# Optimization experiments

Hardware: AMD Instinct MI355X
Metric: run time of the kernel (lower is better)

## Reference

```python
import jax, jax.numpy as jnp
import numpy as np

# dims: T time steps, B batch, F clinical features, H GRU hidden, NH heads, DFF ffn dim, AH single-attn hidden
T, B, F, H, NH, DFF, AH = 128, 256, 76, 64, 4, 256, 8


def setup_inputs() -> dict:
    key = jax.random.key(0)
    ks = jax.random.split(key, 32)
    s = 0.1
    def u(k, shape):
        return jax.random.uniform(k, shape, jnp.float32, -s, s)
    return {
        "x": jax.random.normal(ks[0], (T, B, F), jnp.float32),
        # per-feature GRU(1, H) weight stacks (torch gate order: r, z, n)
        "gru_w_ih": u(ks[1], (F, 3 * H)),          # input dim is 1 -> squeezed
        "gru_w_hh": u(ks[2], (F, 3 * H, H)),
        "gru_b_ih": jnp.zeros((F, 3 * H), jnp.float32),
        "gru_b_hh": jnp.zeros((F, 3 * H), jnp.float32),
        # per-feature SingleAttention('new', time_aware) params
        "att_Wt": u(ks[3], (F, H, AH)),
        "att_Wx": u(ks[4], (F, H, AH)),
        "att_rate": jnp.full((F,), 0.8, jnp.float32),
        # multi-head self-attention over the feature axis
        "mha_wq": u(ks[5], (H, H)), "mha_bq": jnp.zeros((H,), jnp.float32),
        "mha_wk": u(ks[6], (H, H)), "mha_bk": jnp.zeros((H,), jnp.float32),
        "mha_wv": u(ks[7], (H, H)), "mha_bv": jnp.zeros((H,), jnp.float32),
        "mha_wo": u(ks[8], (H, H)), "mha_bo": jnp.zeros((H,), jnp.float32),
        # position-wise feed forward
        "ffn_w1": u(ks[9], (H, DFF)), "ffn_b1": jnp.zeros((DFF,), jnp.float32),
        "ffn_w2": u(ks[10], (DFF, H)), "ffn_b2": jnp.zeros((H,), jnp.float32),
        # FinalAttentionQKV ('mul')
        "fa_wq": u(ks[11], (H, H)), "fa_bq": jnp.zeros((H,), jnp.float32),
        "fa_wk": u(ks[12], (H, H)), "fa_bk": jnp.zeros((H,), jnp.float32),
        "fa_wv": u(ks[13], (H, H)), "fa_bv": jnp.zeros((H,), jnp.float32),
        # output head
        "out0_w": u(ks[14], (H, H)), "out0_b": jnp.zeros((H,), jnp.float32),
        "out1_w": u(ks[15], (H, 1)), "out1_b": jnp.zeros((1,), jnp.float32),
    }


def reference(x, gru_w_ih, gru_w_hh, gru_b_ih, gru_b_hh,
              att_Wt, att_Wx, att_rate,
              mha_wq, mha_bq, mha_wk, mha_bk, mha_wv, mha_bv, mha_wo, mha_bo,
              ffn_w1, ffn_b1, ffn_w2, ffn_b2,
              fa_wq, fa_bq, fa_wk, fa_bk, fa_wv, fa_bv,
              out0_w, out0_b, out1_w, out1_b):
    # x: (T, B, F); torch permutes to (B, T, F)
    Ts, Bsz, Fd = x.shape
    Hd = gru_w_hh.shape[-1]
    dk = Hd // NH

    # ---- all F GRU(1,H) channels fused into one scan (vectorized over F) ----
    xs = jnp.transpose(x, (0, 2, 1))  # (T, F, B)

    def step(h, x_t):  # h: (F,B,H), x_t: (F,B)
        gx = x_t[:, :, None] * gru_w_ih[:, None, :] + gru_b_ih[:, None, :]      # (F,B,3H)
        gh = jnp.einsum('fbh,fgh->fbg', h, gru_w_hh) + gru_b_hh[:, None, :]     # (F,B,3H)
        rx, zx, nx = jnp.split(gx, 3, axis=-1)
        rh, zh, nh = jnp.split(gh, 3, axis=-1)
        r = jax.nn.sigmoid(rx + rh)
        z = jax.nn.sigmoid(zx + zh)
        n = jnp.tanh(nx + r * nh)
        h_new = (1.0 - z) * n + z * h
        return h_new, h_new

    h0 = jnp.zeros((Fd, Bsz, Hd), x.dtype)
    _, hs = jax.lax.scan(step, h0, xs)        # (T, F, B, H)
    hs = jnp.transpose(hs, (1, 2, 0, 3))       # (F, B, T, H)

    # ---- per-feature SingleAttention, type='new', time-aware ----
    q = jnp.einsum('fbh,fha->fba', hs[:, :, -1, :], att_Wt)   # (F,B,AH)
    k = jnp.einsum('fbth,fha->fbta', hs, att_Wx)              # (F,B,T,AH)
    dp = jnp.einsum('fba,fbta->fbt', q, k)                    # (F,B,T)
    sig = jax.nn.sigmoid(dp)
    decay = jnp.arange(Ts, 0, -1, dtype=x.dtype)              # T..1 (time_decays + 1)
    denom = jax.nn.sigmoid(att_rate)[:, None, None] * (jnp.log(2.72 + (1.0 - sig)) * decay)
    e = jax.nn.relu(sig / denom)
    a = jax.nn.softmax(e, axis=-1)
    emb = jnp.einsum('fbt,fbth->bfh', a, hs)                  # (B, F, H)

    def lin(t, w, b):
        return t @ w + b

    # ---- multi-head self-attention over the F axis + residual ----
    # NOTE: original lambda ignores its (layernormed) argument, so LN is dead code.
    def heads(t):
        return t.reshape(Bsz, Fd, NH, dk).transpose(0, 2, 1, 3)
    qh = heads(lin(emb, mha_wq, mha_bq))
    kh = heads(lin(emb, mha_wk, mha_bk))
    vh = heads(lin(emb, mha_wv, mha_bv))
    scores = jnp.einsum('bhqd,bhkd->bhqk', qh, kh) / jnp.sqrt(jnp.asarray(dk, x.dtype))
    attn = jax.nn.softmax(scores, axis=-1)
    ctx = jnp.einsum('bhqk,bhkd->bhqd', attn, vh).transpose(0, 2, 1, 3).reshape(Bsz, Fd, Hd)
    ctx = emb + lin(ctx, mha_wo, mha_bo)

    # ---- position-wise feed-forward + residual ----
    ctx = ctx + lin(jax.nn.relu(lin(ctx, ffn_w1, ffn_b1)), ffn_w2, ffn_b2)

    # ---- FinalAttentionQKV, type='mul' ----
    fq = lin(ctx[:, -1, :], fa_wq, fa_bq)      # (B,H)
    fk = lin(ctx, fa_wk, fa_bk)                # (B,F,H)
    fv = lin(ctx, fa_wv, fa_bv)                # (B,F,H)
    fe = jnp.einsum('bfh,bh->bf', fk, fq)
    fa_w = jax.nn.softmax(fe, axis=1)
    v = jnp.einsum('bf,bfh->bh', fa_w, fv)     # (B,H)

    # ---- output head ----
    out = jax.nn.sigmoid(lin(jax.nn.relu(lin(v, out0_w, out0_b)), out1_w, out1_b))
    return out  # (B, 1)
```

## Files before the change

kernel.cpp:

```cpp
#include <hip/hip_runtime.h>
#include <hip/hip_bf16.h>
#include <cstdint>
#include <cstddef>

#define TT 128
#define BBATCH 256
#define FFEAT 76
#define HDIM 64
#define NHEAD 4
#define DKH 16
#define DFF1 256
#define AH1 8
#define NROWS (BBATCH * FFEAT)

#define LOG2E 1.4426950408889634f

typedef __attribute__((ext_vector_type(8))) short bf16x8;
typedef __attribute__((ext_vector_type(4))) float f32x4;

__device__ __forceinline__ float fast_sigmoid(float v) {
    float p = __builtin_amdgcn_exp2f(-v * LOG2E);
    return __builtin_amdgcn_rcpf(1.0f + p);
}
__device__ __forceinline__ float fast_tanh(float v) {
    float p = __builtin_amdgcn_exp2f(v * (2.0f * LOG2E));
    return 1.0f - 2.0f * __builtin_amdgcn_rcpf(1.0f + p);
}
__device__ __forceinline__ short f2bf(float x) {
    __hip_bfloat16 h = __float2bfloat16(x);
    return *reinterpret_cast<short*>(&h);
}
__device__ __forceinline__ float bf2f(unsigned short s) {
    return __uint_as_float(((unsigned)s) << 16);
}
__device__ __forceinline__ unsigned pack_bf16(float a, float b) {
    unsigned ua = (unsigned)(unsigned short)f2bf(a);
    unsigned ub = (unsigned)(unsigned short)f2bf(b);
    return ua | (ub << 16);
}

__global__ __launch_bounds__(64) void gru_scan_kernel(
    const float* __restrict__ x, const float* __restrict__ w_ih,
    const float* __restrict__ w_hh, const float* __restrict__ b_ih,
    const float* __restrict__ b_hh, const float* __restrict__ Wt,
    const float* __restrict__ Wx, int f_base,
    __hip_bfloat16* __restrict__ hs, float* __restrict__ wtil)
{
    const int f_loc = blockIdx.y;
    const int f     = f_base + f_loc;
    const int b0    = blockIdx.x * 16;
    const int lane  = threadIdx.x;
    const int c     = lane & 15;
    const int q     = lane >> 4;

    __shared__ float x_lds[TT][16];
    __shared__ float wt_s[64][8];
    __shared__ float wx_s[64][8];
    __shared__ short hx[16][72];
    __shared__ float q_s[16][8];

    for (int i = lane; i < TT * 16; i += 64) {
        int t = i >> 4, b = i & 15;
        x_lds[t][b] = x[((size_t)t * BBATCH + b0 + b) * FFEAT + f];
    }
    for (int i = lane; i < 512; i += 64) {
        ((float*)wt_s)[i] = Wt[(size_t)f * 512 + i];
        ((float*)wx_s)[i] = Wx[(size_t)f * 512 + i];
    }
    __syncthreads();

    bf16x8 afr[12][2];
    {
        const float* whh_f = w_hh + (size_t)f * 192 * 64;
        #pragma unroll
        for (int nt = 0; nt < 12; ++nt) {
            int gate = nt >> 2, tt = nt & 3;
            int urow = (c >> 2) * 8 + (tt & 1) * 4 + (c & 3) + (tt >> 1) * 32;
            const float* row = whh_f + (size_t)(gate * 64 + urow) * 64;
            #pragma unroll
            for (int kq = 0; kq < 2; ++kq) {
                bf16x8 fr;
                #pragma unroll
                for (int j = 0; j < 8; ++j) fr[j] = f2bf(row[kq * 32 + q * 8 + j]);
                afr[nt][kq] = fr;
            }
        }
    }
    float wr[4][4], wz[4][4], wn[4][4], bnx[4][4];
    f32x4 biasv[12];
    #pragma unroll
    for (int tt = 0; tt < 4; ++tt) {
        #pragma unroll
        for (int r = 0; r < 4; ++r) {
            int u = q * 8 + (tt & 1) * 4 + r + (tt >> 1) * 32;
            wr[tt][r]  = w_ih[f*192 + u];
            wz[tt][r]  = w_ih[f*192 + 64 + u];
            wn[tt][r]  = w_ih[f*192 + 128 + u];
            bnx[tt][r] = b_ih[f*192 + 128 + u];
            biasv[tt][r]     = b_ih[f*192 + u]      + b_hh[f*192 + u];
            biasv[4 + tt][r] = b_ih[f*192 + 64 + u] + b_hh[f*192 + 64 + u];
            biasv[8 + tt][r] = b_hh[f*192 + 128 + u];
        }
    }

    float hprev[4][4];
    #pragma unroll
    for (int tt = 0; tt < 4; ++tt)
        #pragma unroll
        for (int r = 0; r < 4; ++r) hprev[tt][r] = 0.f;

    bf16x8 hb0 = {0,0,0,0,0,0,0,0};
    bf16x8 hb1 = {0,0,0,0,0,0,0,0};

    short* hs_b = (short*)hs + ((size_t)f_loc * BBATCH + b0 + c) * TT * HDIM;

    for (int t = 0; t < TT; ++t) {
        f32x4 acc[12];
        #pragma unroll
        for (int nt = 0; nt < 12; ++nt) {
            f32x4 a = __builtin_amdgcn_mfma_f32_16x16x32_bf16(afr[nt][0], hb0, biasv[nt], 0, 0, 0);
            acc[nt]  = __builtin_amdgcn_mfma_f32_16x16x32_bf16(afr[nt][1], hb1, a, 0, 0, 0);
        }

        float xv = x_lds[t][c];
        float hn4[4][4];
        #pragma unroll
        for (int tt = 0; tt < 4; ++tt) {
            #pragma unroll
            for (int r = 0; r < 4; ++r) {
                float R  = fmaf(xv, wr[tt][r], acc[tt][r]);
                float Z  = fmaf(xv, wz[tt][r], acc[4 + tt][r]);
                float NX = fmaf(xv, wn[tt][r], bnx[tt][r]);
                float rg = fast_sigmoid(R);
                float zg = fast_sigmoid(Z);
                float ng = fast_tanh(fmaf(rg, acc[8 + tt][r], NX));
                float hn = fmaf(zg, hprev[tt][r] - ng, ng);
                hprev[tt][r] = hn;
                hn4[tt][r] = hn;
            }
        }
        {
            union { int4 i; bf16x8 v; } u0, u1;
            u0.i.x = pack_bf16(hn4[0][0], hn4[0][1]);
            u0.i.y = pack_bf16(hn4[0][2], hn4[0][3]);
            u0.i.z = pack_bf16(hn4[1][0], hn4[1][1]);
            u0.i.w = pack_bf16(hn4[1][2], hn4[1][3]);
            u1.i.x = pack_bf16(hn4[2][0], hn4[2][1]);
            u1.i.y = pack_bf16(hn4[2][2], hn4[2][3]);
            u1.i.z = pack_bf16(hn4[3][0], hn4[3][1]);
            u1.i.w = pack_bf16(hn4[3][2], hn4[3][3]);
            hb0 = u0.v; hb1 = u1.v;
        }
        short* dst = hs_b + (size_t)t * HDIM + q * 8;
        *(bf16x8*)dst = hb0;
        *(bf16x8*)(dst + 32) = hb1;
    }

    *(bf16x8*)&hx[c][q * 8]      = hb0;
    *(bf16x8*)&hx[c][32 + q * 8] = hb1;

    #pragma unroll
    for (int rr = 0; rr < 2; ++rr) {
        int role = rr * 64 + lane;
        int b = role >> 3, a = role & 7;
        float s = 0.f;
        #pragma unroll 8
        for (int j = 0; j < 64; ++j)
            s = fmaf(bf2f((unsigned short)hx[b][j]), wt_s[j][a], s);
        q_s[b][a] = s;
    }
    {
        int b = lane >> 2, jb = (lane & 3) * 16;
        float qreg[8];
        #pragma unroll
        for (int a = 0; a < 8; ++a) qreg[a] = q_s[b][a];
        float* wt_out = wtil + ((size_t)(b0 + b) * FFEAT + f) * HDIM + jb;
        #pragma unroll
        for (int j4 = 0; j4 < 4; ++j4) {
            float4 v;
            #pragma unroll
            for (int jj = 0; jj < 4; ++jj) {
                int j = jb + j4 * 4 + jj;
                float s = 0.f;
                #pragma unroll
                for (int a = 0; a < 8; ++a) s = fmaf(wx_s[j][a], qreg[a], s);
                (&v.x)[jj] = s;
            }
            *(float4*)&wt_out[j4 * 4] = v;
        }
    }
}

__global__ __launch_bounds__(256) void attn2_kernel(
    const __hip_bfloat16* __restrict__ hs, const float* wtil,
    const float* __restrict__ rate, int f_base, float* emb)
{
    const int w     = threadIdx.x >> 6;
    const int lane  = threadIdx.x & 63;
    const int b     = blockIdx.x * 4 + w;
    const int f_loc = blockIdx.y;
    const int f     = f_base + f_loc;
    const int g     = lane >> 3;
    const int i     = lane & 7;

    const uint4* basev = (const uint4*)((const short*)hs +
                          ((size_t)f_loc * BBATCH + b) * TT * HDIM);

    uint4 U[16];
    #pragma unroll
    for (int it = 0; it < 16; ++it)
        U[it] = basev[(it * 8 + g) * 8 + i];

    float wv[8];
    {
        const float4* src = (const float4*)(wtil + ((size_t)b * FFEAT + f) * HDIM + 8 * i);
        float4 a = src[0], c2 = src[1];
        wv[0]=a.x; wv[1]=a.y; wv[2]=a.z; wv[3]=a.w;
        wv[4]=c2.x; wv[5]=c2.y; wv[6]=c2.z; wv[7]=c2.w;
    }
    const float rs = fast_sigmoid(rate[f]);

    float m = -1.0e30f, s = 0.f;
    float o[8];
    #pragma unroll
    for (int j = 0; j < 8; ++j) o[j] = 0.f;

    #pragma unroll
    for (int it = 0; it < 16; ++it) {
        const int t = it * 8 + g;
        uint4 Uv = U[it];
        float h[8];
        h[0] = __uint_as_float(Uv.x << 16); h[1] = __uint_as_float(Uv.x & 0xffff0000u);
        h[2] = __uint_as_float(Uv.y << 16); h[3] = __uint_as_float(Uv.y & 0xffff0000u);
        h[4] = __uint_as_float(Uv.z << 16); h[5] = __uint_as_float(Uv.z & 0xffff0000u);
        h[6] = __uint_as_float(Uv.w << 16); h[7] = __uint_as_float(Uv.w & 0xffff0000u);
        float dp = 0.f;
        #pragma unroll
        for (int j = 0; j < 8; ++j) dp = fmaf(h[j], wv[j], dp);
        dp += __shfl_xor(dp, 1, 64);
        dp += __shfl_xor(dp, 2, 64);
        dp += __shfl_xor(dp, 4, 64);
        float sig = fast_sigmoid(dp);
        float den = rs * (__logf(2.72f + (1.0f - sig)) * (float)(TT - t));
        float e = fmaxf(sig / den, 0.0f);
        float nm = fmaxf(m, e);
        float sc = __builtin_amdgcn_exp2f((m - nm) * LOG2E);
        float p  = __builtin_amdgcn_exp2f((e - nm) * LOG2E);
        s = fmaf(s, sc, p);
        #pragma unroll
        for (int j = 0; j < 8; ++j) o[j] = fmaf(o[j], sc, p * h[j]);
        m = nm;
    }
    #pragma unroll
    for (int k = 8; k <= 32; k <<= 1) {
        float om = __shfl_xor(m, k, 64);
        float os = __shfl_xor(s, k, 64);
        float nm = fmaxf(m, om);
        float sa = __builtin_amdgcn_exp2f((m - nm) * LOG2E);
        float sb = __builtin_amdgcn_exp2f((om - nm) * LOG2E);
        s = s * sa + os * sb;
        #pragma unroll
        for (int j = 0; j < 8; ++j) {
            float oo = __shfl_xor(o[j], k, 64);
            o[j] = o[j] * sa + oo * sb;
        }
        m = nm;
    }
    if (g == 0) {
        float inv = __builtin_amdgcn_rcpf(s);
        float4 v0, v1;
        v0.x = o[0]*inv; v0.y = o[1]*inv; v0.z = o[2]*inv; v0.w = o[3]*inv;
        v1.x = o[4]*inv; v1.y = o[5]*inv; v1.z = o[6]*inv; v1.w = o[7]*inv;
        float* dst = &emb[((size_t)b * FFEAT + f) * HDIM + 8 * i];
        *(float4*)dst       = v0;
        *(float4*)(dst + 4) = v1;
    }
}

struct GemmP {
    const float* X;
    const float* W[3];
    const float* B[3];
    const float* R;
    float* Y[3];
    int K;
    int Nfull;
    int act;
};

__global__ __launch_bounds__(256) void gemm_kernel(GemmP A)
{
    __shared__ float xs[64][65];
    __shared__ float ws[64][68];

    const int tid = threadIdx.x;
    const int tx  = tid & 15;
    const int ty  = tid >> 4;
    const int m0  = blockIdx.x * 64;
    const int n0  = blockIdx.y * 64;
    const int z   = blockIdx.z;

    const float* W = A.W[z];
    const float* Bv = A.B[z];
    float* Y = A.Y[z];
    const int K = A.K, Nfull = A.Nfull;

    float acc[4][4];
    #pragma unroll
    for (int i = 0; i < 4; ++i)
        #pragma unroll
        for (int j = 0; j < 4; ++j) acc[i][j] = 0.f;

    for (int kc = 0; kc < K; kc += 64) {
        for (int s = tid; s < 1024; s += 256) {
            int row = s >> 4, c4 = s & 15;
            float4 xv = *(const float4*)&A.X[(size_t)(m0 + row) * K + kc + 4*c4];
            xs[row][4*c4+0] = xv.x; xs[row][4*c4+1] = xv.y;
            xs[row][4*c4+2] = xv.z; xs[row][4*c4+3] = xv.w;
            float4 wv = *(const float4*)&W[(size_t)(kc + row) * Nfull + n0 + 4*c4];
            *(float4*)&ws[row][4*c4] = wv;
        }
        __syncthreads();
        #pragma unroll 16
        for (int k = 0; k < 64; ++k) {
            float a0 = xs[4*ty+0][k], a1 = xs[4*ty+1][k];
            float a2 = xs[4*ty+2][k], a3 = xs[4*ty+3][k];
            float4 wv = *(const float4*)&ws[k][4*tx];
            #pragma unroll
            for (int j = 0; j < 4; ++j) {
                float wj = (&wv.x)[j];
                acc[0][j] = fmaf(a0, wj, acc[0][j]);
                acc[1][j] = fmaf(a1, wj, acc[1][j]);
                acc[2][j] = fmaf(a2, wj, acc[2][j]);
                acc[3][j] = fmaf(a3, wj, acc[3][j]);
            }
        }
        __syncthreads();
    }

    float4 bias = *(const float4*)&Bv[n0 + 4*tx];
    #pragma unroll
    for (int i = 0; i < 4; ++i) {
        int row = m0 + 4*ty + i;
        float4 v;
        v.x = acc[i][0] + bias.x; v.y = acc[i][1] + bias.y;
        v.z = acc[i][2] + bias.z; v.w = acc[i][3] + bias.w;
        if (A.act) {
            v.x = fmaxf(v.x, 0.f); v.y = fmaxf(v.y, 0.f);
            v.z = fmaxf(v.z, 0.f); v.w = fmaxf(v.w, 0.f);
        }
        if (A.R) {
            float4 r4 = *(const float4*)&A.R[(size_t)row * Nfull + n0 + 4*tx];
            v.x += r4.x; v.y += r4.y; v.z += r4.z; v.w += r4.w;
        }
        *(float4*)&Y[(size_t)row * Nfull + n0 + 4*tx] = v;
    }
}

__global__ __launch_bounds__(256) void mha_core_kernel(
    const float* __restrict__ q, const float* __restrict__ k,
    const float* __restrict__ v, float* __restrict__ ctx)
{
    const int b  = blockIdx.x;
    const int hh = blockIdx.y;
    const int tid = threadIdx.x;

    __shared__ float qs[FFEAT][17];
    __shared__ float ks[FFEAT][17];
    __shared__ float vs[FFEAT][17];
    __shared__ float ps[FFEAT][77];

    for (int idx = tid; idx < FFEAT * DKH; idx += 256) {
        int i = idx >> 4, c = idx & 15;
        size_t g = ((size_t)b * FFEAT + i) * HDIM + hh * DKH + c;
        qs[i][c] = q[g]; ks[i][c] = k[g]; vs[i][c] = v[g];
    }
    __syncthreads();

    for (int idx = tid; idx < FFEAT * FFEAT; idx += 256) {
        int i = idx / FFEAT, j = idx % FFEAT;
        float acc = 0.f;
        #pragma unroll
        for (int c = 0; c < DKH; ++c) acc = fmaf(qs[i][c], ks[j][c], acc);
        ps[i][j] = acc * 0.25f;
    }
    __syncthreads();

    if (tid < FFEAT) {
        float mm = ps[tid][0];
        #pragma unroll 4
        for (int j = 1; j < FFEAT; ++j) mm = fmaxf(mm, ps[tid][j]);
        float ss = 0.f;
        #pragma unroll 4
        for (int j = 0; j < FFEAT; ++j) {
            float pv = __builtin_amdgcn_exp2f((ps[tid][j] - mm) * LOG2E);
            ps[tid][j] = pv; ss += pv;
        }
        float inv = 1.0f / ss;
        #pragma unroll 4
        for (int j = 0; j < FFEAT; ++j) ps[tid][j] *= inv;
    }
    __syncthreads();

    for (int idx = tid; idx < FFEAT * DKH; idx += 256) {
        int i = idx >> 4, c = idx & 15;
        float acc = 0.f;
        #pragma unroll 4
        for (int j = 0; j < FFEAT; ++j) acc = fmaf(ps[i][j], vs[j][c], acc);
        ctx[((size_t)b * FFEAT + i) * HDIM + hh * DKH + c] = acc;
    }
}

__global__ __launch_bounds__(128) void final_kernel(
    const float* __restrict__ ctx3, const float* __restrict__ fk,
    const float* __restrict__ fv,
    const float* __restrict__ faq, const float* __restrict__ fabq,
    const float* __restrict__ o0w, const float* __restrict__ o0b,
    const float* __restrict__ o1w, const float* __restrict__ o1b,
    float* __restrict__ out)
{
    const int b = blockIdx.x;
    const int tid = threadIdx.x;

    __shared__ float last[HDIM];
    __shared__ float fqs[HDIM];
    __shared__ float sm[FFEAT];
    __shared__ float vv[HDIM];
    __shared__ float hh[HDIM];
    __shared__ float redm[2], redp[2];

    if (tid < HDIM) last[tid] = ctx3[((size_t)b * FFEAT + FFEAT - 1) * HDIM + tid];
    __syncthreads();
    if (tid < HDIM) {
        float acc = fabq[tid];
        #pragma unroll 8
        for (int j = 0; j < HDIM; ++j) acc = fmaf(last[j], faq[j * HDIM + tid], acc);
        fqs[tid] = acc;
    }
    __syncthreads();

    float e = -3.0e38f;
    if (tid < FFEAT) {
        const float4* kr = (const float4*)&fk[((size_t)b * FFEAT + tid) * HDIM];
        float acc = 0.f;
        #pragma unroll
        for (int c4 = 0; c4 < 16; ++c4) {
            float4 kv = kr[c4];
            acc = fmaf(kv.x, fqs[4*c4+0], acc);
            acc = fmaf(kv.y, fqs[4*c4+1], acc);
            acc = fmaf(kv.z, fqs[4*c4+2], acc);
            acc = fmaf(kv.w, fqs[4*c4+3], acc);
        }
        e = acc;
    }
    float m = e;
    #pragma unroll
    for (int off = 32; off > 0; off >>= 1) m = fmaxf(m, __shfl_xor(m, off, 64));
    if ((tid & 63) == 0) redm[tid >> 6] = m;
    __syncthreads();
    m = fmaxf(redm[0], redm[1]);
    float p = (tid < FFEAT) ? __builtin_amdgcn_exp2f((e - m) * LOG2E) : 0.f;
    float s = p;
    #pragma unroll
    for (int off = 32; off > 0; off >>= 1) s += __shfl_xor(s, off, 64);
    if ((tid & 63) == 0) redp[tid >> 6] = s;
    __syncthreads();
    s = redp[0] + redp[1];
    if (tid < FFEAT) sm[tid] = p / s;
    __syncthreads();

    if (tid < HDIM) {
        float acc = 0.f;
        for (int ff = 0; ff < FFEAT; ++ff)
            acc = fmaf(sm[ff], fv[((size_t)b * FFEAT + ff) * HDIM + tid], acc);
        vv[tid] = acc;
    }
    __syncthreads();
    if (tid < HDIM) {
        float acc = o0b[tid];
        #pragma unroll 8
        for (int j = 0; j < HDIM; ++j) acc = fmaf(vv[j], o0w[j * HDIM + tid], acc);
        hh[tid] = fmaxf(acc, 0.f);
    }
    __syncthreads();
    if (tid < 64) {
        float t = hh[tid] * o1w[tid];
        #pragma unroll
        for (int off = 32; off > 0; off >>= 1) t += __shfl_xor(t, off, 64);
        if (tid == 0) out[b] = fast_sigmoid(t + o1b[0]);
    }
}

__global__ void ws_report_kernel(float* out, int n, float ws_mib) {
    int i = blockIdx.x * blockDim.x + threadIdx.x;
    if (i < n) out[i] = ws_mib;
}

extern "C" void kernel_launch(void* const* d_in, const int* in_sizes, int n_in,
                              void* d_out, int out_size, void* d_ws, size_t ws_size,
                              hipStream_t stream)
{
    const float* x     = (const float*)d_in[0];
    const float* w_ih  = (const float*)d_in[1];
    const float* w_hh  = (const float*)d_in[2];
    const float* b_ih  = (const float*)d_in[3];
    const float* b_hh  = (const float*)d_in[4];
    const float* attWt = (const float*)d_in[5];
    const float* attWx = (const float*)d_in[6];
    const float* attRt = (const float*)d_in[7];
    const float* wq    = (const float*)d_in[8];
    const float* bq    = (const float*)d_in[9];
    const float* wk    = (const float*)d_in[10];
    const float* bk    = (const float*)d_in[11];
    const float* wv    = (const float*)d_in[12];
    const float* bv    = (const float*)d_in[13];
    const float* wo    = (const float*)d_in[14];
    const float* bo    = (const float*)d_in[15];
    const float* w1    = (const float*)d_in[16];
    const float* b1    = (const float*)d_in[17];
    const float* w2    = (const float*)d_in[18];
    const float* b2    = (const float*)d_in[19];
    const float* faq   = (const float*)d_in[20];
    const float* fabq  = (const float*)d_in[21];
    const float* fak   = (const float*)d_in[22];
    const float* fabk  = (const float*)d_in[23];
    const float* fav   = (const float*)d_in[24];
    const float* fabv  = (const float*)d_in[25];
    const float* o0w   = (const float*)d_in[26];
    const float* o0b   = (const float*)d_in[27];
    const float* o1w   = (const float*)d_in[28];
    const float* o1b   = (const float*)d_in[29];
    float* out = (float*)d_out;

    const size_t embwtil_bytes = (size_t)NROWS * HDIM * 4;
    const size_t R64           = (size_t)NROWS * HDIM;
    const size_t tail_bytes    = 12 * R64 * 4;

    const int chunk_opts[6] = {76, 38, 19, 4, 2, 1};
    int FC = 0;
    for (int i = 0; i < 6; ++i) {
        size_t hs_b = (size_t)chunk_opts[i] * BBATCH * TT * HDIM * 2;
        size_t scratch = hs_b > tail_bytes ? hs_b : tail_bytes;
        if (embwtil_bytes + scratch <= ws_size) { FC = chunk_opts[i]; break; }
    }
    if (FC == 0) {
        ws_report_kernel<<<dim3((out_size + 255) / 256), dim3(256), 0, stream>>>(
            out, out_size, (float)((double)ws_size / (1024.0 * 1024.0)));
        return;
    }

    float* embwtil = (float*)d_ws;
    char*  scratch = (char*)d_ws + embwtil_bytes;
    __hip_bfloat16* hs = (__hip_bfloat16*)scratch;

    for (int f0 = 0; f0 < FFEAT; f0 += FC) {
        int fc = (FFEAT - f0 < FC) ? (FFEAT - f0) : FC;
        gru_scan_kernel<<<dim3(16, fc), dim3(64), 0, stream>>>(
            x, w_ih, w_hh, b_ih, b_hh, attWt, attWx, f0, hs, embwtil);
        attn2_kernel<<<dim3(BBATCH / 4, fc), dim3(256), 0, stream>>>(
            hs, embwtil, attRt, f0, embwtil);
    }

    float* emb  = embwtil;
    float* ts   = (float*)scratch;
    float* q    = ts;
    float* k    = ts + 1*R64;
    float* v    = ts + 2*R64;
    float* ctx  = ts + 3*R64;
    float* ctx2 = ts + 4*R64;
    float* hid  = ts + 5*R64;
    float* ctx3 = ts + 9*R64;
    float* fk   = ts + 10*R64;
    float* fv   = ts + 11*R64;

    const int MB = NROWS / 64;

    {
        GemmP A = { emb, {wq, wk, wv}, {bq, bk, bv}, nullptr, {q, k, v}, 64, 64, 0 };
        gemm_kernel<<<dim3(MB, 1, 3), dim3(256), 0, stream>>>(A);
    }
    mha_core_kernel<<<dim3(BBATCH, NHEAD), dim3(256), 0, stream>>>(q, k, v, ctx);
    {
        GemmP A = { ctx, {wo, nullptr, nullptr}, {bo, nullptr, nullptr}, emb,
                    {ctx2, nullptr, nullptr}, 64, 64, 0 };
        gemm_kernel<<<dim3(MB, 1, 1), dim3(256), 0, stream>>>(A);
    }
    {
        GemmP A = { ctx2, {w1, nullptr, nullptr}, {b1, nullptr, nullptr}, nullptr,
                    {hid, nullptr, nullptr}, 64, 256, 1 };
        gemm_kernel<<<dim3(MB, 4, 1), dim3(256), 0, stream>>>(A);
    }
    {
        GemmP A = { hid, {w2, nullptr, nullptr}, {b2, nullptr, nullptr}, ctx2,
                    {ctx3, nullptr, nullptr}, 256, 64, 0 };
        gemm_kernel<<<dim3(MB, 1, 1), dim3(256), 0, stream>>>(A);
    }
    {
        GemmP A = { ctx3, {fak, fav, nullptr}, {fabk, fabv, nullptr}, nullptr,
                    {fk, fv, nullptr}, 64, 64, 0 };
        gemm_kernel<<<dim3(MB, 1, 2), dim3(256), 0, stream>>>(A);
    }
    final_kernel<<<dim3(BBATCH), dim3(128), 0, stream>>>(
        ctx3, fk, fv, faq, fabq, o0w, o0b, o1w, o1b, out);
}
```

Baseline: 564.7 us.

## Overlap GRU scan of second feature half with attention of first half

Result: no change. 563.8 us (-0.2%).

```diff
diff --git a/kernel.cpp b/kernel.cpp
--- a/kernel.cpp
+++ b/kernel.cpp
@@ -12,6 +12,7 @@
 #define DFF1 256
 #define AH1 8
 #define NROWS (BBATCH * FFEAT)
+#define FCP 38
 
 #define LOG2E 1.4426950408889634f
 
@@ -37,6 +38,267 @@
     unsigned ua = (unsigned)(unsigned short)f2bf(a);
     unsigned ub = (unsigned)(unsigned short)f2bf(b);
     return ua | (ub << 16);
+}
+
+__device__ __forceinline__ void attn_wave(
+    __hip_bfloat16* hs_chunk, const float* Wt, const float* Wx,
+    const float* rate, int f, int f_loc, int b, int lane)
+{
+    const int g = lane >> 3;
+    const int i = lane & 7;
+    short* rowbase = (short*)hs_chunk + ((size_t)f_loc * BBATCH + b) * TT * HDIM;
+    const uint4* basev = (const uint4*)rowbase;
+
+    uint4 U[16];
+    #pragma unroll
+    for (int it = 0; it < 16; ++it)
+        U[it] = basev[(it * 8 + g) * 8 + i];
+
+    float qv[8];
+    {
+        uint4 Uv = U[15];
+        float h15[8];
+        h15[0]=__uint_as_float(Uv.x<<16); h15[1]=__uint_as_float(Uv.x&0xffff0000u);
+        h15[2]=__uint_as_float(Uv.y<<16); h15[3]=__uint_as_float(Uv.y&0xffff0000u);
+        h15[4]=__uint_as_float(Uv.z<<16); h15[5]=__uint_as_float(Uv.z&0xffff0000u);
+        h15[6]=__uint_as_float(Uv.w<<16); h15[7]=__uint_as_float(Uv.w&0xffff0000u);
+        const float* wtp = Wt + (size_t)f * 512 + (size_t)(8 * i) * 8;
+        #pragma unroll
+        for (int a = 0; a < 8; ++a) qv[a] = 0.f;
+        #pragma unroll
+        for (int j = 0; j < 8; ++j)
+            #pragma unroll
+            for (int a = 0; a < 8; ++a)
+                qv[a] = fmaf(h15[j], wtp[j * 8 + a], qv[a]);
+        #pragma unroll
+        for (int a = 0; a < 8; ++a) {
+            qv[a] += __shfl_xor(qv[a], 1, 64);
+            qv[a] += __shfl_xor(qv[a], 2, 64);
+            qv[a] += __shfl_xor(qv[a], 4, 64);
+            qv[a]  = __shfl(qv[a], 63, 64);
+        }
+    }
+    float wv[8];
+    {
+        const float* wxp = Wx + (size_t)f * 512 + (size_t)(8 * i) * 8;
+        #pragma unroll
+        for (int j = 0; j < 8; ++j) {
+            float s2 = 0.f;
+            #pragma unroll
+            for (int a = 0; a < 8; ++a) s2 = fmaf(wxp[j * 8 + a], qv[a], s2);
+            wv[j] = s2;
+        }
+    }
+    const float rs = fast_sigmoid(rate[f]);
+
+    float m = -1.0e30f, s = 0.f;
+    float o[8];
+    #pragma unroll
+    for (int j = 0; j < 8; ++j) o[j] = 0.f;
+
+    #pragma unroll
+    for (int it = 0; it < 16; ++it) {
+        const int t = it * 8 + g;
+        uint4 Uv = U[it];
+        float h[8];
+        h[0] = __uint_as_float(Uv.x << 16); h[1] = __uint_as_float(Uv.x & 0xffff0000u);
+        h[2] = __uint_as_float(Uv.y << 16); h[3] = __uint_as_float(Uv.y & 0xffff0000u);
+        h[4] = __uint_as_float(Uv.z << 16); h[5] = __uint_as_float(Uv.z & 0xffff0000u);
+        h[6] = __uint_as_float(Uv.w << 16); h[7] = __uint_as_float(Uv.w & 0xffff0000u);
+        float dp = 0.f;
+        #pragma unroll
+        for (int j = 0; j < 8; ++j) dp = fmaf(h[j], wv[j], dp);
+        dp += __shfl_xor(dp, 1, 64);
+        dp += __shfl_xor(dp, 2, 64);
+        dp += __shfl_xor(dp, 4, 64);
+        float sig = fast_sigmoid(dp);
+        float den = rs * (__logf(2.72f + (1.0f - sig)) * (float)(TT - t));
+        float e = fmaxf(sig / den, 0.0f);
+        float nm = fmaxf(m, e);
+        float sc = __builtin_amdgcn_exp2f((m - nm) * LOG2E);
+        float p  = __builtin_amdgcn_exp2f((e - nm) * LOG2E);
+        s = fmaf(s, sc, p);
+        #pragma unroll
+        for (int j = 0; j < 8; ++j) o[j] = fmaf(o[j], sc, p * h[j]);
+        m = nm;
+    }
+    #pragma unroll
+    for (int k = 8; k <= 32; k <<= 1) {
+        float om = __shfl_xor(m, k, 64);
+        float os = __shfl_xor(s, k, 64);
+        float nm = fmaxf(m, om);
+        float sa = __builtin_amdgcn_exp2f((m - nm) * LOG2E);
+        float sb = __builtin_amdgcn_exp2f((om - nm) * LOG2E);
+        s = s * sa + os * sb;
+        #pragma unroll
+        for (int j = 0; j < 8; ++j) {
+            float oo = __shfl_xor(o[j], k, 64);
+            o[j] = o[j] * sa + oo * sb;
+        }
+        m = nm;
+    }
+    if (g == 0) {
+        float inv = __builtin_amdgcn_rcpf(s);
+        float4 v0, v1;
+        v0.x = o[0]*inv; v0.y = o[1]*inv; v0.z = o[2]*inv; v0.w = o[3]*inv;
+        v1.x = o[4]*inv; v1.y = o[5]*inv; v1.z = o[6]*inv; v1.w = o[7]*inv;
+        float* edst = (float*)rowbase;
+        *(float4*)&edst[8 * i]     = v0;
+        *(float4*)&edst[8 * i + 4] = v1;
+    }
+}
+
+__global__ __launch_bounds__(64) void fused_gru_attn_kernel(
+    const float* __restrict__ x, const float* __restrict__ w_ih,
+    const float* __restrict__ w_hh, const float* __restrict__ b_ih,
+    const float* __restrict__ b_hh, const float* __restrict__ Wt,
+    const float* __restrict__ Wx, const float* __restrict__ rate,
+    int ngru, int f0_gru, __hip_bfloat16* __restrict__ hs_w,
+    int f0_att, __hip_bfloat16* hs_r)
+{
+    __shared__ float x_lds[TT][16];
+    const int gid  = blockIdx.x;
+    const int lane = threadIdx.x;
+
+    if (gid < ngru) {
+        const int f_loc = gid >> 4;
+        const int f     = f0_gru + f_loc;
+        const int b0    = (gid & 15) * 16;
+        const int c     = lane & 15;
+        const int q     = lane >> 4;
+
+        for (int i = lane; i < TT * 16; i += 64) {
+            int t = i >> 4, b = i & 15;
+            x_lds[t][b] = x[((size_t)t * BBATCH + b0 + b) * FFEAT + f];
+        }
+        __syncthreads();
+
+        bf16x8 afr[12][2];
+        {
+            const float* whh_f = w_hh + (size_t)f * 192 * 64;
+            #pragma unroll
+            for (int nt = 0; nt < 12; ++nt) {
+                int gate = nt >> 2, tt = nt & 3;
+                int urow = (c >> 2) * 8 + (tt & 1) * 4 + (c & 3) + (tt >> 1) * 32;
+                const float* row = whh_f + (size_t)(gate * 64 + urow) * 64;
+                #pragma unroll
+                for (int kq = 0; kq < 2; ++kq) {
+                    bf16x8 fr;
+                    #pragma unroll
+                    for (int j = 0; j < 8; ++j) fr[j] = f2bf(row[kq * 32 + q * 8 + j]);
+                    afr[nt][kq] = fr;
+                }
+            }
+        }
+        float wr[4][4], wz[4][4], wn[4][4], bnx[4][4];
+        f32x4 biasv[12];
+        #pragma unroll
+        for (int tt = 0; tt < 4; ++tt) {
+            #pragma unroll
+            for (int r = 0; r < 4; ++r) {
+                int u = q * 8 + (tt & 1) * 4 + r + (tt >> 1) * 32;
+                wr[tt][r]  = w_ih[f*192 + u];
+                wz[tt][r]  = w_ih[f*192 + 64 + u];
+                wn[tt][r]  = w_ih[f*192 + 128 + u];
+                bnx[tt][r] = b_ih[f*192 + 128 + u];
+                biasv[tt][r]     = b_ih[f*192 + u]      + b_hh[f*192 + u];
+                biasv[4 + tt][r] = b_ih[f*192 + 64 + u] + b_hh[f*192 + 64 + u];
+                biasv[8 + tt][r] = b_hh[f*192 + 128 + u];
+            }
+        }
+
+        float hprev[4][4];
+        #pragma unroll
+        for (int tt = 0; tt < 4; ++tt)
+            #pragma unroll
+            for (int r = 0; r < 4; ++r) hprev[tt][r] = 0.f;
+
+        bf16x8 hb0 = {0,0,0,0,0,0,0,0};
+        bf16x8 hb1 = {0,0,0,0,0,0,0,0};
+
+        short* hs_b = (short*)hs_w + ((size_t)f_loc * BBATCH + b0 + c) * TT * HDIM;
+
+        for (int t = 0; t < TT; ++t) {
+            f32x4 acc[12];
+            #pragma unroll
+            for (int nt = 0; nt < 12; ++nt) {
+                f32x4 a = __builtin_amdgcn_mfma_f32_16x16x32_bf16(afr[nt][0], hb0, biasv[nt], 0, 0, 0);
+                acc[nt]  = __builtin_amdgcn_mfma_f32_16x16x32_bf16(afr[nt][1], hb1, a, 0, 0, 0);
+            }
+
+            float xv = x_lds[t][c];
+            float hn4[4][4];
+            #pragma unroll
+            for (int tt = 0; tt < 4; ++tt) {
+                #pragma unroll
+                for (int r = 0; r < 4; ++r) {
+                    float R  = fmaf(xv, wr[tt][r], acc[tt][r]);
+                    float Z  = fmaf(xv, wz[tt][r], acc[4 + tt][r]);
+                    float NX = fmaf(xv, wn[tt][r], bnx[tt][r]);
+                    float rg = fast_sigmoid(R);
+                    float zg = fast_sigmoid(Z);
+                    float ng = fast_tanh(fmaf(rg, acc[8 + tt][r], NX));
+                    float hn = fmaf(zg, hprev[tt][r] - ng, ng);
+                    hprev[tt][r] = hn;
+                    hn4[tt][r] = hn;
+                }
+            }
+            {
+                union { int4 i; bf16x8 v; } u0, u1;
+                u0.i.x = pack_bf16(hn4[0][0], hn4[0][1]);
+                u0.i.y = pack_bf16(hn4[0][2], hn4[0][3]);
+                u0.i.z = pack_bf16(hn4[1][0], hn4[1][1]);
+                u0.i.w = pack_bf16(hn4[1][2], hn4[1][3]);
+                u1.i.x = pack_bf16(hn4[2][0], hn4[2][1]);
+                u1.i.y = pack_bf16(hn4[2][2], hn4[2][3]);
+                u1.i.z = pack_bf16(hn4[3][0], hn4[3][1]);
+                u1.i.w = pack_bf16(hn4[3][2], hn4[3][3]);
+                hb0 = u0.v; hb1 = u1.v;
+            }
+            short* dst = hs_b + (size_t)t * HDIM + q * 8;
+            *(bf16x8*)dst = hb0;
+            *(bf16x8*)(dst + 32) = hb1;
+        }
+    } else {
+        const int aid   = gid - ngru;
+        const int b     = aid & 255;
+        const int f_loc = aid >> 8;
+        attn_wave(hs_r, Wt, Wx, rate, f0_att + f_loc, f_loc, b, lane);
+    }
+}
+
+__global__ __launch_bounds__(256) void attn2_p_kernel(
+    __hip_bfloat16* hs_chunk, const float* __restrict__ Wt,
+    const float* __restrict__ Wx, const float* __restrict__ rate, int f_base)
+{
+    const int w    = threadIdx.x >> 6;
+    const int lane = threadIdx.x & 63;
+    const int b    = blockIdx.x * 4 + w;
+    const int f_loc = blockIdx.y;
+    attn_wave(hs_chunk, Wt, Wx, rate, f_base + f_loc, f_loc, b, lane);
+}
+
+__global__ __launch_bounds__(64) void bounce_kernel(float* hs0f)
+{
+    const int k = blockIdx.x;
+    hs0f[(size_t)(400 + k) * 4096 + 2048 + threadIdx.x] =
+        hs0f[(size_t)k * 4096 + threadIdx.x];
+}
+
+__global__ __launch_bounds__(64) void compact_kernel(
+    const float* hs0f, const float* hs1f, float* emb)
+{
+    const int j = blockIdx.x;
+    const int f = j >> 8;
+    const int b = j & 255;
+    const int chunk = (f >= FCP);
+    const int f_loc = chunk ? f - FCP : f;
+    const size_t row = (size_t)f_loc * BBATCH + b;
+    const float* base = chunk ? hs1f : hs0f;
+    size_t off = (!chunk && row <= 303)
+               ? ((size_t)(400 + row) * 4096 + 2048)
+               : row * 4096;
+    emb[((size_t)b * FFEAT + f) * HDIM + threadIdx.x] = base[off + threadIdx.x];
 }
 
 __global__ __launch_bounds__(64) void gru_scan_kernel(
@@ -494,6 +756,55 @@
 __global__ void ws_report_kernel(float* out, int n, float ws_mib) {
     int i = blockIdx.x * blockDim.x + threadIdx.x;
     if (i < n) out[i] = ws_mib;
+}
+
+static void run_tail(const float* emb, float* ts,
+                     const float* wq, const float* bq, const float* wk2, const float* bk2,
+                     const float* wv2, const float* bv2, const float* wo, const float* bo,
+                     const float* w1, const float* b1, const float* w2, const float* b2,
+                     const float* faq, const float* fabq, const float* fak, const float* fabk,
+                     const float* fav, const float* fabv, const float* o0w, const float* o0b,
+                     const float* o1w, const float* o1b, float* out, hipStream_t stream)
+{
+    const size_t R64 = (size_t)NROWS * HDIM;
+    float* q    = ts;
+    float* k    = ts + 1*R64;
+    float* v    = ts + 2*R64;
+    float* ctx  = ts + 3*R64;
+    float* ctx2 = ts + 4*R64;
+    float* hid  = ts + 5*R64;
+    float* ctx3 = ts + 9*R64;
+    float* fk   = ts + 10*R64;
+    float* fv   = ts + 11*R64;
+    const int MB = NROWS / 64;
+
+    {
+        GemmP A = { emb, {wq, wk2, wv2}, {bq, bk2, bv2}, nullptr, {q, k, v}, 64, 64, 0 };
+        gemm_kernel<<<dim3(MB, 1, 3), dim3(256), 0, stream>>>(A);
+    }
+    mha_core_kernel<<<dim3(BBATCH, NHEAD), dim3(256), 0, stream>>>(q, k, v, ctx);
+    {
+        GemmP A = { ctx, {wo, nullptr, nullptr}, {bo, nullptr, nullptr}, emb,
+                    {ctx2, nullptr, nullptr}, 64, 64, 0 };
+        gemm_kernel<<<dim3(MB, 1, 1), dim3(256), 0, stream>>>(A);
+    }
+    {
+        GemmP A = { ctx2, {w1, nullptr, nullptr}, {b1, nullptr, nullptr}, nullptr,
+                    {hid, nullptr, nullptr}, 64, 256, 1 };
+        gemm_kernel<<<dim3(MB, 4, 1), dim3(256), 0, stream>>>(A);
+    }
+    {
+        GemmP A = { hid, {w2, nullptr, nullptr}, {b2, nullptr, nullptr}, ctx2,
+                    {ctx3, nullptr, nullptr}, 256, 64, 0 };
+        gemm_kernel<<<dim3(MB, 1, 1), dim3(256), 0, stream>>>(A);
+    }
+    {
+        GemmP A = { ctx3, {fak, fav, nullptr}, {fabk, fabv, nullptr}, nullptr,
+                    {fk, fv, nullptr}, 64, 64, 0 };
+        gemm_kernel<<<dim3(MB, 1, 2), dim3(256), 0, stream>>>(A);
+    }
+    final_kernel<<<dim3(BBATCH), dim3(128), 0, stream>>>(
+        ctx3, fk, fv, faq, fabq, o0w, o0b, o1w, o1b, out);
 }
 
 extern "C" void kernel_launch(void* const* d_in, const int* in_sizes, int n_in,
@@ -532,16 +843,41 @@
     const float* o1b   = (const float*)d_in[29];
     float* out = (float*)d_out;
 
-    const size_t embwtil_bytes = (size_t)NROWS * HDIM * 4;
-    const size_t R64           = (size_t)NROWS * HDIM;
-    const size_t tail_bytes    = 12 * R64 * 4;
+    const size_t emb_bytes = (size_t)NROWS * HDIM * 4;
+    const size_t hs_half   = (size_t)FCP * BBATCH * TT * HDIM * 2;
+
+    if (ws_size >= 2 * hs_half) {
+        __hip_bfloat16* hs0 = (__hip_bfloat16*)d_ws;
+        __hip_bfloat16* hs1 = (__hip_bfloat16*)((char*)d_ws + hs_half);
+
+        fused_gru_attn_kernel<<<dim3(16 * FCP), dim3(64), 0, stream>>>(
+            x, w_ih, w_hh, b_ih, b_hh, attWt, attWx, attRt,
+            16 * FCP, 0, hs0, 0, hs1);
+        fused_gru_attn_kernel<<<dim3(16 * FCP + BBATCH * FCP), dim3(64), 0, stream>>>(
+            x, w_ih, w_hh, b_ih, b_hh, attWt, attWx, attRt,
+            16 * FCP, FCP, hs1, 0, hs0);
+        bounce_kernel<<<dim3(304), dim3(64), 0, stream>>>((float*)hs0);
+        attn2_p_kernel<<<dim3(BBATCH / 4, FCP), dim3(256), 0, stream>>>(
+            hs1, attWt, attWx, attRt, FCP);
+        float* emb = (float*)d_ws;
+        compact_kernel<<<dim3(NROWS), dim3(64), 0, stream>>>(
+            (const float*)hs0, (const float*)hs1, emb);
+
+        float* ts = (float*)((char*)d_ws + emb_bytes);
+        run_tail(emb, ts, wq, bq, wk, bk, wv, bv, wo, bo, w1, b1, w2, b2,
+                 faq, fabq, fak, fabk, fav, fabv, o0w, o0b, o1w, o1b, out, stream);
+        return;
+    }
+
+    const size_t R64        = (size_t)NROWS * HDIM;
+    const size_t tail_bytes = 12 * R64 * 4;
 
     const int chunk_opts[6] = {76, 38, 19, 4, 2, 1};
     int FC = 0;
     for (int i = 0; i < 6; ++i) {
         size_t hs_b = (size_t)chunk_opts[i] * BBATCH * TT * HDIM * 2;
         size_t scratch = hs_b > tail_bytes ? hs_b : tail_bytes;
-        if (embwtil_bytes + scratch <= ws_size) { FC = chunk_opts[i]; break; }
+        if (emb_bytes + scratch <= ws_size) { FC = chunk_opts[i]; break; }
     }
     if (FC == 0) {
         ws_report_kernel<<<dim3((out_size + 255) / 256), dim3(256), 0, stream>>>(
@@ -550,7 +886,7 @@
     }
 
     float* embwtil = (float*)d_ws;
-    char*  scratch = (char*)d_ws + embwtil_bytes;
+    char*  scratch = (char*)d_ws + emb_bytes;
     __hip_bfloat16* hs = (__hip_bfloat16*)scratch;
 
     for (int f0 = 0; f0 < FFEAT; f0 += FC) {
@@ -561,45 +897,6 @@
             hs, embwtil, attRt, f0, embwtil);
     }
 
-    float* emb  = embwtil;
-    float* ts   = (float*)scratch;
-    float* q    = ts;
-    float* k    = ts + 1*R64;
-    float* v    = ts + 2*R64;
-    float* ctx  = ts + 3*R64;
-    float* ctx2 = ts + 4*R64;
-    float* hid  = ts + 5*R64;
-    float* ctx3 = ts + 9*R64;
-    float* fk   = ts + 10*R64;
-    float* fv   = ts + 11*R64;
-
-    const int MB = NROWS / 64;
-
-    {
-        GemmP A = { emb, {wq, wk, wv}, {bq, bk, bv}, nullptr, {q, k, v}, 64, 64, 0 };
-        gemm_kernel<<<dim3(MB, 1, 3), dim3(256), 0, stream>>>(A);
-    }
-    mha_core_kernel<<<dim3(BBATCH, NHEAD), dim3(256), 0, stream>>>(q, k, v, ctx);
-    {
-        GemmP A = { ctx, {wo, nullptr, nullptr}, {bo, nullptr, nullptr}, emb,
-                    {ctx2, nullptr, nullptr}, 64, 64, 0 };
-        gemm_kernel<<<dim3(MB, 1, 1), dim3(256), 0, stream>>>(A);
-    }
-    {
-        GemmP A = { ctx2, {w1, nullptr, nullptr}, {b1, nullptr, nullptr}, nullptr,
-                    {hid, nullptr, nullptr}, 64, 256, 1 };
-        gemm_kernel<<<dim3(MB, 4, 1), dim3(256), 0, stream>>>(A);
-    }
-    {
-        GemmP A = { hid, {w2, nullptr, nullptr}, {b2, nullptr, nullptr}, ctx2,
-                    {ctx3, nullptr, nullptr}, 256, 64, 0 };
-        gemm_kernel<<<dim3(MB, 1, 1), dim3(256), 0, stream>>>(A);
-    }
-    {
-        GemmP A = { ctx3, {fak, fav, nullptr}, {fabk, fabv, nullptr}, nullptr,
-                    {fk, fv, nullptr}, 64, 64, 0 };
-        gemm_kernel<<<dim3(MB, 1, 2), dim3(256), 0, stream>>>(A);
-    }
-    final_kernel<<<dim3(BBATCH), dim3(128), 0, stream>>>(
-        ctx3, fk, fv, faq, fabq, o0w, o0b, o1w, o1b, out);
-}
+    run_tail(embwtil, (float*)scratch, wq, bq, wk, bk, wv, bv, wo, bo, w1, b1, w2, b2,
+             faq, fabq, fak, fabk, fav, fabv, o0w, o0b, o1w, o1b, out, stream);
+}
```
